# Kernel tuning notes

Hardware: AMD Instinct MI355X
Metric: run time of the kernel (lower is better)

Reference implementation:

```python
import jax, jax.numpy as jnp
import numpy as np

EMBED_DIM = 1024
NUM_HEADS = 16
HEAD_DIM = EMBED_DIM // NUM_HEADS
B, S = 2, 2048


def setup_inputs() -> dict:
    key = jax.random.key(0)
    ks = jax.random.split(key, 9)
    s = 1.0 / np.sqrt(EMBED_DIM)
    return {
        "x": jax.random.normal(ks[0], (B, S, EMBED_DIM), dtype=jnp.float32),
        "Wq": jax.random.normal(ks[1], (EMBED_DIM, EMBED_DIM), dtype=jnp.float32) * s,
        "bq": jnp.zeros((EMBED_DIM,), dtype=jnp.float32),
        "Wk": jax.random.normal(ks[2], (EMBED_DIM, EMBED_DIM), dtype=jnp.float32) * s,
        "bk": jnp.zeros((EMBED_DIM,), dtype=jnp.float32),
        "Wv": jax.random.normal(ks[3], (EMBED_DIM, EMBED_DIM), dtype=jnp.float32) * s,
        "bv": jnp.zeros((EMBED_DIM,), dtype=jnp.float32),
        "Wo": jax.random.normal(ks[4], (EMBED_DIM, EMBED_DIM), dtype=jnp.float32) * s,
        "bo": jnp.zeros((EMBED_DIM,), dtype=jnp.float32),
    }


def reference(x, Wq, bq, Wk, bk, Wv, bv, Wo, bo):
    b, s, _ = x.shape
    # Projections; reshape to [B, H, S, Dh]
    def proj(W, bias):
        return (x @ W + bias).reshape(b, s, NUM_HEADS, HEAD_DIM).transpose(0, 2, 1, 3)
    q = proj(Wq, bq)
    k = proj(Wk, bk)
    v = proj(Wv, bv)
    scale = 1.0 / np.sqrt(HEAD_DIM).astype(np.float32)
    scores = jnp.einsum('bhqd,bhkd->bhqk', q, k) * scale  # [B,H,S,S]
    attn = jax.nn.softmax(scores, axis=-1)
    out = jnp.einsum('bhqk,bhkd->bhqd', attn, v)  # [B,H,S,Dh]
    out = out.transpose(0, 2, 1, 3).reshape(b, s, EMBED_DIM)
    return out @ Wo + bo
```

## Files before the change

### kernel.cpp

```cpp
#include <hip/hip_runtime.h>
#include <hip/hip_bf16.h>

typedef unsigned short ushort_t;
typedef __attribute__((ext_vector_type(8))) short short8;
typedef __attribute__((ext_vector_type(4))) float f32x4;
typedef __attribute__((ext_vector_type(16))) float f32x16;
typedef __attribute__((ext_vector_type(2))) unsigned int uint2v;

#define EMBED 1024
#define NHEAD 16
#define HDIM 64
#define BB 2
#define SSEQ 2048
#define MROWS (BB*SSEQ)
#define QKV_N (3*EMBED)
#define PER_BUF (MROWS*EMBED)

__device__ __forceinline__ ushort_t f2bf(float f) {
    union { float f; unsigned int u; } x; x.f = f;
    unsigned int r = x.u + 0x7fffu + ((x.u >> 16) & 1u);
    return (ushort_t)(r >> 16);
}
__device__ __forceinline__ unsigned cvt_pk_bf16(float lo, float hi) {
    unsigned r;
    asm("v_cvt_pk_bf16_f32 %0, %1, %2" : "=v"(r) : "v"(lo), "v"(hi));
    return r;
}

__device__ __forceinline__ void gload16(const void* g, void* l) {
    __builtin_amdgcn_global_load_lds(
        (const __attribute__((address_space(1))) unsigned int*)g,
        (__attribute__((address_space(3))) unsigned int*)l, 16, 0, 0);
}

__global__ void cast_bf16_kernel(const float* __restrict__ in, ushort_t* __restrict__ out, int n) {
    int i = (blockIdx.x * blockDim.x + threadIdx.x) * 4;
    if (i + 3 < n) {
        float4 v = *(const float4*)(in + i);
        out[i+0] = f2bf(v.x); out[i+1] = f2bf(v.y);
        out[i+2] = f2bf(v.z); out[i+3] = f2bf(v.w);
    }
}

__global__ void transpose_cast4_kernel(
    const float* __restrict__ W0, const float* __restrict__ W1,
    const float* __restrict__ W2, const float* __restrict__ W3,
    ushort_t* __restrict__ T0, ushort_t* __restrict__ T1,
    ushort_t* __restrict__ T2, ushort_t* __restrict__ T3)
{
    __shared__ float tile[32][33];
    int z = blockIdx.z;
    const float* W = (z == 0) ? W0 : (z == 1) ? W1 : (z == 2) ? W2 : W3;
    ushort_t* Wt   = (z == 0) ? T0 : (z == 1) ? T1 : (z == 2) ? T2 : T3;
    int tx = threadIdx.x, ty = threadIdx.y;
    int n0 = blockIdx.x * 32, k0 = blockIdx.y * 32;
    #pragma unroll
    for (int i = 0; i < 4; i++)
        tile[ty*4+i][tx] = W[(size_t)(k0 + ty*4 + i) * EMBED + n0 + tx];
    __syncthreads();
    #pragma unroll
    for (int i = 0; i < 4; i++)
        Wt[(size_t)(n0 + ty*4 + i) * EMBED + k0 + tx] = f2bf(tile[tx][ty*4+i]);
}

__global__ void transpose_v_kernel(const ushort_t* __restrict__ v, ushort_t* __restrict__ vt) {
    __shared__ ushort_t tile[64][66];
    int bh = blockIdx.y, s0 = blockIdx.x * 64;
    int t = threadIdx.x;
    int r = t >> 3, c8 = (t & 7) * 8;
    #pragma unroll
    for (int p = 0; p < 2; p++) {
        short8 vv = *(const short8*)&v[((size_t)bh*SSEQ + s0 + p*32 + r)*HDIM + c8];
        #pragma unroll
        for (int j = 0; j < 8; j++) tile[p*32 + r][c8 + j] = (ushort_t)vv[j];
    }
    __syncthreads();
    #pragma unroll
    for (int p = 0; p < 2; p++) {
        int d = p*32 + r;
        short8 ov;
        #pragma unroll
        for (int j = 0; j < 8; j++) ov[j] = (short)tile[c8 + j][d];
        *(short8*)&vt[((size_t)bh*HDIM + d)*SSEQ + s0 + c8] = ov;
    }
}

template<int OUT_MODE>
__global__ __launch_bounds__(256) void gemm_bt_kernel(
    const ushort_t* __restrict__ A,
    const ushort_t* __restrict__ Bt,
    const float* __restrict__ b0, const float* __restrict__ b1, const float* __restrict__ b2,
    void* __restrict__ Cout,
    int M, int N, int K)
{
    __shared__ __attribute__((aligned(16))) ushort_t Asm[128*32];
    __shared__ __attribute__((aligned(16))) ushort_t Bsm[128*32];
    int t = threadIdx.x;
    int w = t >> 6, l = t & 63;
    int wr = w >> 1, wc = w & 1;
    int lrow = l & 15, lhi = l >> 4;

    int gx = gridDim.x;
    int flat = blockIdx.y * gx + blockIdx.x;
    int q8 = (gx * gridDim.y) >> 3;
    int nf = (flat & 7) * q8 + (flat >> 3);
    int m0 = (nf / gx) * 128, n0 = (nf % gx) * 128;

    int srow = l >> 2;
    int scol = (l & 3) * 8;

    f32x4 acc[4][4];
    #pragma unroll
    for (int mi = 0; mi < 4; mi++)
        #pragma unroll
        for (int ni = 0; ni < 4; ni++)
            #pragma unroll
            for (int c = 0; c < 4; c++) acc[mi][ni][c] = 0.f;

    for (int k0 = 0; k0 < K; k0 += 32) {
        __syncthreads();
        #pragma unroll
        for (int p = 0; p < 2; p++) {
            gload16(&A [(size_t)(m0 + w*32 + p*16 + srow)*K + k0 + scol], &Asm[(w*32 + p*16)*32]);
            gload16(&Bt[(size_t)(n0 + w*32 + p*16 + srow)*K + k0 + scol], &Bsm[(w*32 + p*16)*32]);
        }
        __syncthreads();
        short8 af[4], bfr[4];
        #pragma unroll
        for (int mi = 0; mi < 4; mi++)
            af[mi] = *(short8*)&Asm[(wr*64 + mi*16 + lrow)*32 + lhi*8];
        #pragma unroll
        for (int ni = 0; ni < 4; ni++)
            bfr[ni] = *(short8*)&Bsm[(wc*64 + ni*16 + lrow)*32 + lhi*8];
        __builtin_amdgcn_s_setprio(1);
        #pragma unroll
        for (int mi = 0; mi < 4; mi++)
            #pragma unroll
            for (int ni = 0; ni < 4; ni++)
                acc[mi][ni] = __builtin_amdgcn_mfma_f32_16x16x32_bf16(af[mi], bfr[ni], acc[mi][ni], 0, 0, 0);
        __builtin_amdgcn_s_setprio(0);
    }

    #pragma unroll
    for (int mi = 0; mi < 4; mi++)
        #pragma unroll
        for (int ni = 0; ni < 4; ni++) {
            int col = n0 + wc*64 + ni*16 + lrow;
            #pragma unroll
            for (int c = 0; c < 4; c++) {
                int row = m0 + wr*64 + mi*16 + lhi*4 + c;
                if (OUT_MODE == 0) {
                    float v = acc[mi][ni][c] + b0[col];
                    ((float*)Cout)[(size_t)row * N + col] = v;
                } else {
                    int which = col >> 10, hc = col & 1023;
                    const float* bp = (which == 0) ? b0 : (which == 1) ? b1 : b2;
                    float v = acc[mi][ni][c] + bp[hc];
                    if (which == 0) v *= 0.18033688011112042f;
                    int h = hc >> 6, d = hc & 63;
                    int b = row >> 11, s = row & 2047;
                    ((ushort_t*)Cout)[(size_t)which*PER_BUF + ((size_t)((b*NHEAD + h)*SSEQ) + s)*HDIM + d] = f2bf(v);
                }
            }
        }
}

#define MFMA32(a,b,c) __builtin_amdgcn_mfma_f32_32x32x16_bf16(a, b, c, 0, 0, 0)

__global__ __launch_bounds__(256, 2) void flash_attn2_kernel(
    const ushort_t* __restrict__ q,
    const ushort_t* __restrict__ k,
    const ushort_t* __restrict__ vt,
    ushort_t* __restrict__ o)
{
    __shared__ __attribute__((aligned(16))) ushort_t Ks[2][64*64];
    __shared__ __attribute__((aligned(16))) ushort_t Vs[2][64*64];

    int t = threadIdx.x, w = t >> 6, l = t & 63;
    int l31 = l & 31, hi = l >> 5;

    int flat = blockIdx.x;
    int wg = (flat & 7) * 64 + (flat >> 3);
    int bh = wg >> 4;
    int q0 = (wg & 15) * 128;

    const ushort_t* qp = q  + (size_t)bh * SSEQ * HDIM;
    const ushort_t* kp = k  + (size_t)bh * SSEQ * HDIM;
    const ushort_t* vp = vt + (size_t)bh * HDIM * SSEQ;

    int lr = l >> 3, lc = l & 7;
    int colel = 8 * (lc ^ lr);

    short8 qf[4];
    int qrow = q0 + w*32 + l31;
    #pragma unroll
    for (int st = 0; st < 4; st++)
        qf[st] = *(const short8*)&qp[(size_t)qrow*HDIM + st*16 + hi*8];

    f32x16 o0 = {}, o1 = {};
    float m_run = -1e30f, l_run = 0.f;

    #define STAGE(buf, kv0) { \
        _Pragma("unroll") \
        for (int c = 0; c < 2; c++) { \
            int row = w*16 + c*8 + lr; \
            gload16(&kp[(size_t)(kv0 + row)*HDIM + colel], &Ks[buf][(w*16 + c*8)*64]); \
            gload16(&vp[(size_t)row*SSEQ + (kv0) + colel], &Vs[buf][(w*16 + c*8)*64]); \
        } }

    STAGE(0, 0)
    asm volatile("s_waitcnt vmcnt(0)");
    __syncthreads();
    int cur = 0;

    for (int kv0 = 0; kv0 < SSEQ; kv0 += 64) {
        if (kv0 + 64 < SSEQ) { STAGE(cur ^ 1, kv0 + 64) }

        f32x16 s0 = {}, s1 = {};
        __builtin_amdgcn_s_setprio(1);
        #pragma unroll
        for (int st = 0; st < 4; st++) {
            int colb = st*16 + hi*8;
            short8 kf0 = *(const short8*)&Ks[cur][l31*64        + (colb ^ ((l31 & 7) << 3))];
            short8 kf1 = *(const short8*)&Ks[cur][(32 + l31)*64 + (colb ^ ((l31 & 7) << 3))];
            s0 = MFMA32(kf0, qf[st], s0);
            s1 = MFMA32(kf1, qf[st], s1);
        }
        __builtin_amdgcn_s_setprio(0);

        float ma = fmaxf(s0[0], s0[1]);
        float mb = fmaxf(s0[2], s0[3]);
        float mc = fmaxf(s0[4], s0[5]);
        float md = fmaxf(s0[6], s0[7]);
        ma = fmaxf(fmaxf(ma, s0[8]),  s0[9]);
        mb = fmaxf(fmaxf(mb, s0[10]), s0[11]);
        mc = fmaxf(fmaxf(mc, s0[12]), s0[13]);
        md = fmaxf(fmaxf(md, s0[14]), s0[15]);
        ma = fmaxf(fmaxf(ma, s1[0]),  s1[1]);
        mb = fmaxf(fmaxf(mb, s1[2]),  s1[3]);
        mc = fmaxf(fmaxf(mc, s1[4]),  s1[5]);
        md = fmaxf(fmaxf(md, s1[6]),  s1[7]);
        ma = fmaxf(fmaxf(ma, s1[8]),  s1[9]);
        mb = fmaxf(fmaxf(mb, s1[10]), s1[11]);
        mc = fmaxf(fmaxf(mc, s1[12]), s1[13]);
        md = fmaxf(fmaxf(md, s1[14]), s1[15]);
        float mx = fmaxf(fmaxf(ma, mb), fmaxf(mc, md));
        mx = fmaxf(mx, __shfl_xor(mx, 32));

        if (__any(mx > m_run + 8.f)) {
            float mnew = fmaxf(m_run, mx);
            float alpha = __builtin_amdgcn_exp2f(m_run - mnew);
            #pragma unroll
            for (int r = 0; r < 16; r++) { o0[r] *= alpha; o1[r] *= alpha; }
            l_run *= alpha;
            m_run = mnew;
        }
        float r0 = 0.f, r1 = 0.f, r2 = 0.f, r3 = 0.f;
        #pragma unroll
        for (int r = 0; r < 16; r += 4) {
            s0[r]   = __builtin_amdgcn_exp2f(s0[r]   - m_run); r0 += s0[r];
            s0[r+1] = __builtin_amdgcn_exp2f(s0[r+1] - m_run); r1 += s0[r+1];
            s0[r+2] = __builtin_amdgcn_exp2f(s0[r+2] - m_run); r2 += s0[r+2];
            s0[r+3] = __builtin_amdgcn_exp2f(s0[r+3] - m_run); r3 += s0[r+3];
        }
        #pragma unroll
        for (int r = 0; r < 16; r += 4) {
            s1[r]   = __builtin_amdgcn_exp2f(s1[r]   - m_run); r0 += s1[r];
            s1[r+1] = __builtin_amdgcn_exp2f(s1[r+1] - m_run); r1 += s1[r+1];
            s1[r+2] = __builtin_amdgcn_exp2f(s1[r+2] - m_run); r2 += s1[r+2];
            s1[r+3] = __builtin_amdgcn_exp2f(s1[r+3] - m_run); r3 += s1[r+3];
        }
        float rs = (r0 + r1) + (r2 + r3);
        rs += __shfl_xor(rs, 32);
        l_run += rs;

        short8 pfr[4];
        #pragma unroll
        for (int kt = 0; kt < 2; kt++) {
            #pragma unroll
            for (int sub = 0; sub < 2; sub++) {
                const f32x16& sv = (kt == 0) ? s0 : s1;
                int b8 = sub * 8;
                unsigned a0 = cvt_pk_bf16(sv[b8+0], sv[b8+1]);
                unsigned a1 = cvt_pk_bf16(sv[b8+2], sv[b8+3]);
                unsigned b0 = cvt_pk_bf16(sv[b8+4], sv[b8+5]);
                unsigned b1 = cvt_pk_bf16(sv[b8+6], sv[b8+7]);
                uint2v rr0 = __builtin_amdgcn_permlane32_swap(a0, b0, false, false);
                uint2v rr1 = __builtin_amdgcn_permlane32_swap(a1, b1, false, false);
                union { unsigned u[4]; short8 v; } pf;
                pf.u[0] = rr0.x; pf.u[1] = rr1.x; pf.u[2] = rr0.y; pf.u[3] = rr1.y;
                pfr[kt*2 + sub] = pf.v;
            }
        }

        __builtin_amdgcn_s_setprio(1);
        #pragma unroll
        for (int ks = 0; ks < 4; ks++) {
            int colb = ks*16 + hi*8;
            short8 vf0 = *(const short8*)&Vs[cur][l31*64        + (colb ^ ((l31 & 7) << 3))];
            short8 vf1 = *(const short8*)&Vs[cur][(32 + l31)*64 + (colb ^ ((l31 & 7) << 3))];
            o0 = MFMA32(vf0, pfr[ks], o0);
            o1 = MFMA32(vf1, pfr[ks], o1);
        }
        __builtin_amdgcn_s_setprio(0);

        asm volatile("s_waitcnt vmcnt(0)");
        __syncthreads();
        cur ^= 1;
    }

    float rl = 1.f / l_run;
    ushort_t* Ot = ((ushort_t*)Ks) + w*(32*64);
    #pragma unroll
    for (int dt = 0; dt < 2; dt++)
        #pragma unroll
        for (int rq = 0; rq < 4; rq++) {
            float v0 = (dt ? o1[rq*4+0] : o0[rq*4+0]) * rl;
            float v1 = (dt ? o1[rq*4+1] : o0[rq*4+1]) * rl;
            float v2 = (dt ? o1[rq*4+2] : o0[rq*4+2]) * rl;
            float v3 = (dt ? o1[rq*4+3] : o0[rq*4+3]) * rl;
            int d0 = dt*32 + rq*8 + hi*4;
            uint2v pw = { cvt_pk_bf16(v0, v1), cvt_pk_bf16(v2, v3) };
            *(uint2v*)&Ot[l31*64 + (d0 ^ ((l31 & 7) << 3))] = pw;
        }

    int b = bh >> 4, h = bh & 15;
    int q2 = l >> 1, dh = (l & 1) * 32;
    size_t obase = ((size_t)(b*SSEQ) + q0 + w*32 + q2)*EMBED + h*HDIM;
    #pragma unroll
    for (int j = 0; j < 4; j++) {
        int d = dh + j*8;
        short8 ov = *(short8*)&Ot[q2*64 + (d ^ ((q2 & 7) << 3))];
        *(short8*)&o[obase + d] = ov;
    }
}

extern "C" void kernel_launch(void* const* d_in, const int* in_sizes, int n_in,
                              void* d_out, int out_size, void* d_ws, size_t ws_size,
                              hipStream_t stream) {
    const float* x  = (const float*)d_in[0];
    const float* Wq = (const float*)d_in[1];
    const float* bq = (const float*)d_in[2];
    const float* Wk = (const float*)d_in[3];
    const float* bk = (const float*)d_in[4];
    const float* Wv = (const float*)d_in[5];
    const float* bv = (const float*)d_in[6];
    const float* Wo = (const float*)d_in[7];
    const float* bo = (const float*)d_in[8];

    char* ws = (char*)d_ws;
    ushort_t* xb  = (ushort_t*)(ws);
    ushort_t* WqT = (ushort_t*)(ws + (8u  << 20));
    ushort_t* WkT = (ushort_t*)(ws + (10u << 20));
    ushort_t* WvT = (ushort_t*)(ws + (12u << 20));
    ushort_t* WoT = (ushort_t*)(ws + (14u << 20));
    ushort_t* qb  = (ushort_t*)(ws + (16u << 20));
    ushort_t* kb  = (ushort_t*)(ws + (24u << 20));
    ushort_t* vb  = (ushort_t*)(ws + (32u << 20));
    ushort_t* vtb = (ushort_t*)(ws + (40u << 20));
    ushort_t* ab  = xb;

    int nx = MROWS * EMBED;
    cast_bf16_kernel<<<nx/(256*4), 256, 0, stream>>>(x, xb, nx);

    transpose_cast4_kernel<<<dim3(EMBED/32, EMBED/32, 4), dim3(32, 8), 0, stream>>>(
        Wq, Wk, Wv, Wo, WqT, WkT, WvT, WoT);

    gemm_bt_kernel<2><<<dim3(QKV_N/128, MROWS/128), 256, 0, stream>>>(
        xb, WqT, bq, bk, bv, qb, MROWS, QKV_N, EMBED);

    transpose_v_kernel<<<dim3(SSEQ/64, BB*NHEAD), 256, 0, stream>>>(vb, vtb);

    flash_attn2_kernel<<<512, 256, 0, stream>>>(qb, kb, vtb, ab);

    gemm_bt_kernel<0><<<dim3(EMBED/128, MROWS/128), 256, 0, stream>>>(
        ab, WoT, bo, bo, bo, d_out, MROWS, EMBED, EMBED);
}
```

Baseline: 132.8 us.

## Split attention KV range in two halves and merge with a combine kernel

The flash-attention launch now splits the key/value sequence into two halves, each handled by its own workgroup via a second grid dimension. Each half writes a bf16 partial output and a per-row log-sum-exp to scratch buffers that reuse dead workspace and the output buffer. A new combine kernel reweights the two partials and writes the head-interleaved layout the output projection expects. Launch bounds are raised to allow more resident workgroups, aiming for better CU occupancy and latency hiding. The cost is an extra kernel, extra memory traffic for the partials, and some precision loss from storing bf16 partials.

```diff
diff --git a/kernel.cpp b/kernel.cpp
--- a/kernel.cpp
+++ b/kernel.cpp
@@ -15,11 +15,16 @@
 #define MROWS (BB*SSEQ)
 #define QKV_N (3*EMBED)
 #define PER_BUF (MROWS*EMBED)
+#define NROWS_BH (BB*NHEAD*SSEQ)
 
 __device__ __forceinline__ ushort_t f2bf(float f) {
     union { float f; unsigned int u; } x; x.f = f;
     unsigned int r = x.u + 0x7fffu + ((x.u >> 16) & 1u);
     return (ushort_t)(r >> 16);
+}
+__device__ __forceinline__ float bf2f(ushort_t u) {
+    union { unsigned int u; float f; } x; x.u = ((unsigned int)u) << 16;
+    return x.f;
 }
 __device__ __forceinline__ unsigned cvt_pk_bf16(float lo, float hi) {
     unsigned r;
@@ -167,11 +172,13 @@
 
 #define MFMA32(a,b,c) __builtin_amdgcn_mfma_f32_32x32x16_bf16(a, b, c, 0, 0, 0)
 
-__global__ __launch_bounds__(256, 2) void flash_attn2_kernel(
+__global__ __launch_bounds__(256, 4) void flash_attn2_kernel(
     const ushort_t* __restrict__ q,
     const ushort_t* __restrict__ k,
     const ushort_t* __restrict__ vt,
-    ushort_t* __restrict__ o)
+    ushort_t* __restrict__ on0,
+    ushort_t* __restrict__ on1,
+    float* __restrict__ Lbuf)
 {
     __shared__ __attribute__((aligned(16))) ushort_t Ks[2][64*64];
     __shared__ __attribute__((aligned(16))) ushort_t Vs[2][64*64];
@@ -183,6 +190,8 @@
     int wg = (flat & 7) * 64 + (flat >> 3);
     int bh = wg >> 4;
     int q0 = (wg & 15) * 128;
+    int half = blockIdx.y;
+    int kvbeg = half << 10;
 
     const ushort_t* qp = q  + (size_t)bh * SSEQ * HDIM;
     const ushort_t* kp = k  + (size_t)bh * SSEQ * HDIM;
@@ -208,13 +217,13 @@
             gload16(&vp[(size_t)row*SSEQ + (kv0) + colel], &Vs[buf][(w*16 + c*8)*64]); \
         } }
 
-    STAGE(0, 0)
+    STAGE(0, kvbeg)
     asm volatile("s_waitcnt vmcnt(0)");
     __syncthreads();
     int cur = 0;
 
-    for (int kv0 = 0; kv0 < SSEQ; kv0 += 64) {
-        if (kv0 + 64 < SSEQ) { STAGE(cur ^ 1, kv0 + 64) }
+    for (int kv0 = kvbeg; kv0 < kvbeg + 1024; kv0 += 64) {
+        if (kv0 + 64 < kvbeg + 1024) { STAGE(cur ^ 1, kv0 + 64) }
 
         f32x16 s0 = {}, s1 = {};
         __builtin_amdgcn_s_setprio(1);
@@ -324,15 +333,43 @@
             *(uint2v*)&Ot[l31*64 + (d0 ^ ((l31 & 7) << 3))] = pw;
         }
 
-    int b = bh >> 4, h = bh & 15;
+    if (hi == 0)
+        Lbuf[(size_t)half*NROWS_BH + (size_t)bh*SSEQ + q0 + w*32 + l31] = m_run + __log2f(l_run);
+
+    ushort_t* On = half ? on1 : on0;
     int q2 = l >> 1, dh = (l & 1) * 32;
-    size_t obase = ((size_t)(b*SSEQ) + q0 + w*32 + q2)*EMBED + h*HDIM;
+    size_t obase = ((size_t)bh*SSEQ + q0 + w*32 + q2)*HDIM;
     #pragma unroll
     for (int j = 0; j < 4; j++) {
         int d = dh + j*8;
         short8 ov = *(short8*)&Ot[q2*64 + (d ^ ((q2 & 7) << 3))];
-        *(short8*)&o[obase + d] = ov;
-    }
+        *(short8*)&On[obase + d] = ov;
+    }
+}
+
+__global__ void combine_kernel(const ushort_t* __restrict__ on0,
+                               const ushort_t* __restrict__ on1,
+                               const float* __restrict__ Lbuf,
+                               ushort_t* __restrict__ o)
+{
+    int idx = blockIdx.x * 256 + threadIdx.x;
+    int row = idx >> 3;
+    int c8 = (idx & 7) * 8;
+    float L0 = Lbuf[row], L1 = Lbuf[NROWS_BH + row];
+    float Lm = fmaxf(L0, L1);
+    float w0 = __builtin_amdgcn_exp2f(L0 - Lm);
+    float w1 = __builtin_amdgcn_exp2f(L1 - Lm);
+    float rinv = 1.f / (w0 + w1);
+    w0 *= rinv; w1 *= rinv;
+    short8 a = *(const short8*)&on0[(size_t)row*HDIM + c8];
+    short8 b = *(const short8*)&on1[(size_t)row*HDIM + c8];
+    short8 out;
+    #pragma unroll
+    for (int j = 0; j < 8; j++)
+        out[j] = (short)f2bf(w0*bf2f((ushort_t)a[j]) + w1*bf2f((ushort_t)b[j]));
+    int bh = row >> 11, s = row & 2047;
+    int bb = bh >> 4, h = bh & 15;
+    *(short8*)&o[((size_t)(bb*SSEQ + s))*EMBED + h*HDIM + c8] = out;
 }
 
 extern "C" void kernel_launch(void* const* d_in, const int* in_sizes, int n_in,
@@ -360,6 +397,10 @@
     ushort_t* vtb = (ushort_t*)(ws + (40u << 20));
     ushort_t* ab  = xb;
 
+    ushort_t* on0  = vb;
+    ushort_t* on1  = (ushort_t*)d_out;
+    float*    Lbuf = (float*)(ws + (8u << 20));
+
     int nx = MROWS * EMBED;
     cast_bf16_kernel<<<nx/(256*4), 256, 0, stream>>>(x, xb, nx);
 
@@ -371,7 +412,9 @@
 
     transpose_v_kernel<<<dim3(SSEQ/64, BB*NHEAD), 256, 0, stream>>>(vb, vtb);
 
-    flash_attn2_kernel<<<512, 256, 0, stream>>>(qb, kb, vtb, ab);
+    flash_attn2_kernel<<<dim3(512, 2), 256, 0, stream>>>(qb, kb, vtb, on0, on1, Lbuf);
+
+    combine_kernel<<<(NROWS_BH*8)/256, 256, 0, stream>>>(on0, on1, Lbuf, ab);
 
     gemm_bt_kernel<0><<<dim3(EMBED/128, MROWS/128), 256, 0, stream>>>(
         ab, WoT, bo, bo, bo, d_out, MROWS, EMBED, EMBED);
```

New measurement: 135.5 us. +2.1%, slower.
